# Kernel optimization log

Measured on AMD Instinct MI355X. Metric: run time of the kernel, lower is better.

The kernel has to match this reference:

```python
import jax, jax.numpy as jnp
import numpy as np

N = 50000
E = 800000
D = 256        # encoder_dim; also hidden*heads for both layers
H = 4          # heads
C = 64         # hidden_dim per head
OUT = 5        # classes
NEG_SLOPE = 0.2
GN_EPS = 1e-5
SM_EPS = 1e-16  # PyG softmax denominator epsilon


def setup_inputs() -> dict:
    key = jax.random.key(0)
    ks = jax.random.split(key, 20)
    sc = lambda fan_in: 1.0 / np.sqrt(fan_in)
    inp = {
        "x": jax.random.normal(ks[0], (N, D), dtype=jnp.float32),
        "edge_index": jax.random.randint(ks[1], (2, E), 0, N, dtype=jnp.int64),
        # two GATv2 layers (stacked on leading axis): lin_l, lin_r, att, bias
        "Wl": jax.random.normal(ks[2], (2, D, H * C), dtype=jnp.float32) * sc(D),
        "Wr": jax.random.normal(ks[3], (2, D, H * C), dtype=jnp.float32) * sc(D),
        "att": jax.random.normal(ks[4], (2, H, C), dtype=jnp.float32) * sc(C),
        "bconv": jnp.zeros((2, H * C), dtype=jnp.float32),
        # parallel linear skips
        "Wlin": jax.random.normal(ks[5], (2, D, H * C), dtype=jnp.float32) * sc(D),
        "blin": jnp.zeros((2, H * C), dtype=jnp.float32),
        # GraphNorm params
        "gn_w": jnp.ones((2, H * C), dtype=jnp.float32),
        "gn_b": jnp.zeros((2, H * C), dtype=jnp.float32),
        "gn_ms": jnp.ones((2, H * C), dtype=jnp.float32),
        # final GATv2 (concat=False -> head mean, out=5) and final linear
        "fWl": jax.random.normal(ks[6], (D, H * OUT), dtype=jnp.float32) * sc(D),
        "fWr": jax.random.normal(ks[7], (D, H * OUT), dtype=jnp.float32) * sc(D),
        "fatt": jax.random.normal(ks[8], (H, OUT), dtype=jnp.float32) * sc(OUT),
        "fbconv": jnp.zeros((OUT,), dtype=jnp.float32),
        "fWlin": jax.random.normal(ks[9], (D, OUT), dtype=jnp.float32) * sc(D),
        "fblin": jnp.zeros((OUT,), dtype=jnp.float32),
    }
    return inp


def _gatv2(x, src, dst, Wl, Wr, att, heads, ch):
    # x: [N, Din]; returns [N, heads, ch]
    n = x.shape[0]
    xl = (x @ Wl).reshape(n, heads, ch)  # source messages
    xr = (x @ Wr).reshape(n, heads, ch)  # target query part
    e = jax.nn.leaky_relu(xl[src] + xr[dst], NEG_SLOPE)      # [E, H, C]
    score = jnp.einsum("ehc,hc->eh", e, att)                  # [E, H]
    # segment softmax over incoming edges of each target node
    m = jax.ops.segment_max(score, dst, num_segments=n)       # [N, H]
    a = jnp.exp(score - m[dst])
    denom = jax.ops.segment_sum(a, dst, num_segments=n)       # [N, H]
    alpha = a / (denom[dst] + SM_EPS)                         # [E, H]
    return jax.ops.segment_sum(alpha[..., None] * xl[src], dst, num_segments=n)


def _graphnorm(x, w, b, ms):
    mean = jnp.mean(x, axis=0)
    centered = x - mean * ms
    var = jnp.mean(centered * centered, axis=0)
    return w * centered * jax.lax.rsqrt(var + GN_EPS) + b


def reference(x, edge_index, Wl, Wr, att, bconv, Wlin, blin, gn_w, gn_b, gn_ms,
              fWl, fWr, fatt, fbconv, fWlin, fblin):
    src, dst = edge_index[0], edge_index[1]
    emb = x
    for i in range(2):
        cpart = _gatv2(emb, src, dst, Wl[i], Wr[i], att[i], H, C).reshape(N, H * C) + bconv[i]
        lpart = emb @ Wlin[i] + blin[i]
        cpart = _graphnorm(cpart, gn_w[i], gn_b[i], gn_ms[i])
        emb = jax.nn.elu(cpart + lpart)
    cpart = _gatv2(emb, src, dst, fWl, fWr, fatt, H, OUT).mean(axis=1) + fbconv  # concat=False
    lpart = emb @ fWlin + fblin
    return jax.nn.log_softmax(cpart + lpart, axis=1)
```

## Files before the change

kernel.cpp:

```cpp
#include <hip/hip_runtime.h>

#define NN 50000
#define EE 800000
#define DD 256
#define NB 196

typedef unsigned short u16;
typedef unsigned int u32;

typedef __attribute__((ext_vector_type(8))) short short8;
typedef __attribute__((ext_vector_type(4))) float f32x4;
typedef __attribute__((ext_vector_type(4))) unsigned short u16x4;

__device__ __forceinline__ float b2f(u16 u) {
  union { u32 i; float f; } c; c.i = ((u32)u) << 16; return c.f;
}
__device__ __forceinline__ u16 f2b(float f) {
  union { float f; u32 i; } c; c.f = f;
  u32 u = c.i;
  return (u16)((u + 0x7fffu + ((u >> 16) & 1u)) >> 16);
}
__device__ __forceinline__ float lrelu(float x) { return fmaxf(x, 0.2f * x); }
__device__ __forceinline__ float ldf(const void* p, int i, int bf) {
  return bf ? b2f(((const u16*)p)[i]) : ((const float*)p)[i];
}
__device__ __forceinline__ int lde(const void* ei, int idx, int m64) {
  int v = m64 ? (int)((const long long*)ei)[idx] : ((const int*)ei)[idx];
  return v < 0 ? 0 : (v >= NN ? NN - 1 : v);
}
__device__ __forceinline__ float cexp(float s) {
  return __expf(fminf(fmaxf(s, -60.f), 60.f));
}

__global__ __launch_bounds__(256) void init_kernel(const void* x, const void* ei,
                                                   int* flags, int* cnt) {
  int i = blockIdx.x * 256 + threadIdx.x;
  if (i < NN) cnt[i] = 0;
  if (blockIdx.x == 0 && threadIdx.x < 64) {
    int lane = threadIdx.x;
    const u16* xw = (const u16*)x;
    int c = 0;
    for (int k = lane; k < 512; k += 64) {
      u16 w = xw[k];
      int e = (w >> 7) & 0xFF;
      if ((e >= 107 && e <= 147) || (w & 0x7FFF) == 0) ++c;
    }
    const u32* ew = (const u32*)ei;
    int zc = 0;
    for (int k = 1 + 2 * lane; k < 1024; k += 128)
      if (ew[k] == 0) ++zc;
    #pragma unroll
    for (int off = 1; off < 64; off <<= 1) {
      c += __shfl_xor(c, off);
      zc += __shfl_xor(zc, off);
    }
    if (lane == 0) {
      flags[0] = (c >= 440) ? 1 : 0;
      flags[1] = (zc >= 400) ? 1 : 0;
    }
  }
}

__global__ void hist_kernel(const void* ei, const int* flags, int* cnt) {
  int e = blockIdx.x * 256 + threadIdx.x;
  if (e < EE) atomicAdd(&cnt[lde(ei, EE + e, flags[1])], 1);
}

__global__ __launch_bounds__(256) void bsum_kernel(const int* __restrict__ deg,
                                                   int* __restrict__ bsum) {
  int i = blockIdx.x * 256 + threadIdx.x;
  int v = (i < NN) ? deg[i] : 0;
  #pragma unroll
  for (int off = 1; off < 64; off <<= 1) v += __shfl_xor(v, off);
  __shared__ int ws[4];
  int lane = threadIdx.x & 63, wid = threadIdx.x >> 6;
  if (lane == 0) ws[wid] = v;
  __syncthreads();
  if (threadIdx.x == 0) bsum[blockIdx.x] = ws[0] + ws[1] + ws[2] + ws[3];
}

__global__ __launch_bounds__(256) void bscan_kernel(const int* __restrict__ bsum,
                                                    int* __restrict__ boff) {
  int t = threadIdx.x;
  int v = (t < NB) ? bsum[t] : 0;
  int iv = v;
  int lane = t & 63, wid = t >> 6;
  #pragma unroll
  for (int off = 1; off < 64; off <<= 1) {
    int u = __shfl_up(iv, off);
    if (lane >= off) iv += u;
  }
  __shared__ int ws[4];
  if (lane == 63) ws[wid] = iv;
  __syncthreads();
  int add = 0;
  for (int w = 0; w < wid; ++w) add += ws[w];
  if (t < NB) boff[t] = iv - v + add;
}

__global__ __launch_bounds__(256) void bwrite_kernel(const int* __restrict__ deg,
                                                     const int* __restrict__ boff,
                                                     int* __restrict__ rowptr) {
  int i = blockIdx.x * 256 + threadIdx.x;
  int v = (i < NN) ? deg[i] : 0;
  int iv = v;
  int lane = threadIdx.x & 63, wid = threadIdx.x >> 6;
  #pragma unroll
  for (int off = 1; off < 64; off <<= 1) {
    int u = __shfl_up(iv, off);
    if (lane >= off) iv += u;
  }
  __shared__ int ws[4];
  if (lane == 63) ws[wid] = iv;
  __syncthreads();
  int add = boff[blockIdx.x];
  for (int w = 0; w < wid; ++w) add += ws[w];
  if (i <= NN) rowptr[i] = iv - v + add;
}

__global__ void fill_kernel(const void* ei, const int* flags, const int* __restrict__ rowptr,
                            int* __restrict__ cnt, int* __restrict__ col) {
  int e = blockIdx.x * 256 + threadIdx.x;
  if (e < EE) {
    int m64 = flags[1];
    int dst = lde(ei, EE + e, m64);
    int old = atomicSub(&cnt[dst], 1);
    int pos = rowptr[dst] + old - 1;
    if (pos >= 0 && pos < EE) col[pos] = lde(ei, e, m64);
  }
}

__global__ __launch_bounds__(256) void prep_kernel(
    const void* Wl, const void* Wr, const void* Wlin,
    const void* fWl, const void* fWr, const void* fWlin,
    const void* x, const int* flags, u16* wpack, u16* fwp, u16* xb) {
  int bf = flags[0];
  int bid = blockIdx.x;
  if (bid < 1536) {
    int idx = bid * 256 + threadIdx.x;
    int m = idx >> 16, e = idx & 65535;
    int layer = (m >= 3) ? 1 : 0, sel = m - layer * 3;
    const void* src = (sel == 0 ? Wl : (sel == 1 ? Wr : Wlin));
    int k = e >> 8, n = e & 255;
    wpack[(m << 16) + ((((k >> 3) << 8) + n) << 3) + (k & 7)] =
        f2b(ldf(src, layer * 65536 + e, bf));
  } else if (bid < 1584) {
    int idx = (bid - 1536) * 256 + threadIdx.x;
    int j = idx & 7;
    int col = (idx >> 3) % 48;
    int kk = idx / (48 * 8);
    int k = kk * 8 + j;
    float v = 0.f;
    if (col < 20)      v = ldf(fWl, k * 20 + col, bf);
    else if (col < 40) v = ldf(fWr, k * 20 + (col - 20), bf);
    else if (col < 45) v = ldf(fWlin, k * 5 + (col - 40), bf);
    fwp[idx] = f2b(v);
  } else {
    int base = (bid - 1584) * 1024 + threadIdx.x * 4;
    if (bf) {
      *(u16x4*)(xb + base) = *(const u16x4*)((const u16*)x + base);
    } else {
      f32x4 s = *(const f32x4*)((const float*)x + base);
      u16x4 o;
      #pragma unroll
      for (int j = 0; j < 4; ++j) o[j] = f2b(s[j]);
      *(u16x4*)(xb + base) = o;
    }
  }
}

__global__ __launch_bounds__(256) void gemm_kernel(
    const u16* __restrict__ A, const u16* __restrict__ wpack, const void* blin,
    const int* flags, int layer, float* __restrict__ sums,
    u16* __restrict__ xl, u16* __restrict__ xr, u16* __restrict__ lp, int M) {
  __shared__ __align__(16) u16 bsh[16384];
  if (blockIdx.x == 0 && blockIdx.y == 0) {
    sums[threadIdx.x] = 0.f;
    sums[threadIdx.x + 256] = 0.f;
  }
  int wave = threadIdx.x >> 6;
  int lane = threadIdx.x & 63;
  int q = lane >> 4;
  int t = lane & 15;
  int m0 = blockIdx.x * 64 + wave * 16;
  int yh = blockIdx.y;

  int arow = m0 + t;
  if (arow >= M) arow = M - 1;
  const u16* Abase = A + (size_t)arow * DD + q * 8;
  short8 af[8];
  #pragma unroll
  for (int i = 0; i < 8; ++i) af[i] = *(const short8*)(Abase + i * 32);

  int bf = flags[0];

  for (int yi = 0; yi < 6; ++yi) {
    int y = yh * 6 + yi;
    int m = y >> 2;
    int col0 = (y & 3) * 64;
    const u16* wb = wpack + (m << 16);

    __syncthreads();
    #pragma unroll
    for (int itc = 0; itc < 8; ++itc) {
      int chunk = threadIdx.x + itc * 256;
      int kk = chunk >> 6;
      int off = chunk & 63;
      *(uint4*)&bsh[(kk << 9) + (off << 3)] =
          *(const uint4*)(wb + (((kk << 8) + col0) << 3) + (off << 3));
    }
    __syncthreads();

    f32x4 acc[4];
    #pragma unroll
    for (int ns = 0; ns < 4; ++ns) acc[ns] = (f32x4){0.f, 0.f, 0.f, 0.f};

    #pragma unroll
    for (int i = 0; i < 8; ++i) {
      int kk = i * 4 + q;
      const u16* bb = &bsh[(kk << 9) + (t << 3)];
      #pragma unroll
      for (int ns = 0; ns < 4; ++ns) {
        short8 b = *(const short8*)(bb + (ns << 7));
        acc[ns] = __builtin_amdgcn_mfma_f32_16x16x32_bf16(af[i], b, acc[ns], 0, 0, 0);
      }
    }

    u16* dstp = (y < 4) ? xl : (y < 8) ? xr : lp;
    bool isLp = (y >= 8);
    #pragma unroll
    for (int ns = 0; ns < 4; ++ns) {
      int c = col0 + ns * 16 + t;
      float bias = isLp ? ldf(blin, layer * 256 + c, bf) : 0.f;
      #pragma unroll
      for (int r = 0; r < 4; ++r) {
        int row = m0 + q * 4 + r;
        if (row < M) dstp[(size_t)row * DD + c] = f2b(acc[ns][r] + bias);
      }
    }
  }
}

__global__ __launch_bounds__(256) void fgemm_kernel(
    const u16* __restrict__ A, const u16* __restrict__ fwp, const void* fblin,
    const int* flags, float* __restrict__ zl, float* __restrict__ zr,
    float* __restrict__ lp5, int M) {
  int wave = threadIdx.x >> 6;
  int lane = threadIdx.x & 63;
  int q = lane >> 4;
  int t = lane & 15;
  int m0 = blockIdx.x * 64 + wave * 16;

  f32x4 acc[3];
  #pragma unroll
  for (int ns = 0; ns < 3; ++ns) acc[ns] = (f32x4){0.f, 0.f, 0.f, 0.f};

  int arow = m0 + t;
  if (arow >= M) arow = M - 1;
  const u16* Abase = A + (size_t)arow * DD + q * 8;

  #pragma unroll
  for (int k0 = 0; k0 < DD; k0 += 32) {
    short8 a = *(const short8*)(Abase + k0);
    int kk = (k0 >> 3) + q;
    #pragma unroll
    for (int ns = 0; ns < 3; ++ns) {
      short8 b = *(const short8*)(fwp + (((kk * 48) + ns * 16 + t) << 3));
      acc[ns] = __builtin_amdgcn_mfma_f32_16x16x32_bf16(a, b, acc[ns], 0, 0, 0);
    }
  }

  int bf = flags[0];
  #pragma unroll
  for (int ns = 0; ns < 3; ++ns) {
    int c = ns * 16 + t;
    #pragma unroll
    for (int r = 0; r < 4; ++r) {
      int row = m0 + q * 4 + r;
      if (row < M) {
        float v = acc[ns][r];
        if (c < 20)      zl[row * 20 + c] = v;
        else if (c < 40) zr[row * 20 + (c - 20)] = v;
        else if (c < 45) lp5[row * 5 + (c - 40)] = v + ldf(fblin, c - 40, bf);
      }
    }
  }
}

__device__ __forceinline__ void edge_step(u16x4 s4, const float* xrv, const float* atv,
                                          float& l, float* acc) {
  float x0 = b2f(s4[0]), x1 = b2f(s4[1]), x2 = b2f(s4[2]), x3 = b2f(s4[3]);
  float sp = atv[0] * lrelu(x0 + xrv[0]) + atv[1] * lrelu(x1 + xrv[1]) +
             atv[2] * lrelu(x2 + xrv[2]) + atv[3] * lrelu(x3 + xrv[3]);
  sp += __shfl_xor(sp, 1);
  sp += __shfl_xor(sp, 2);
  sp += __shfl_xor(sp, 4);
  sp += __shfl_xor(sp, 8);
  float pz = cexp(sp);
  l += pz;
  acc[0] += pz * x0;
  acc[1] += pz * x1;
  acc[2] += pz * x2;
  acc[3] += pz * x3;
}

__global__ __launch_bounds__(256) void agg_kernel(
    const u16* __restrict__ xl, const u16* __restrict__ xr,
    const int* __restrict__ rowptr, const int* __restrict__ col,
    const void* att, const void* bconv, const int* flags, int layer,
    u16* __restrict__ cpart) {
  int wave = threadIdx.x >> 6;
  int node = blockIdx.x * 4 + wave;
  int lane = threadIdx.x & 63;
  int h = lane >> 4;
  int cb = (lane & 15) * 4;
  int base = h * 64 + cb;
  int bf = flags[0];

  u16x4 r4 = *(const u16x4*)(xr + (size_t)node * DD + base);
  float xrv[4], atv[4];
  #pragma unroll
  for (int j = 0; j < 4; ++j) {
    xrv[j] = b2f(r4[j]);
    atv[j] = ldf(att, layer * 256 + base + j, bf);
  }

  float l = 0.f;
  float acc[4] = {0.f, 0.f, 0.f, 0.f};
  int e0 = rowptr[node], e1 = rowptr[node + 1];
  const u16* xlp = xl + base;

  int e = e0;
  for (; e + 4 <= e1; e += 4) {
    int s0 = col[e], s1 = col[e + 1], s2 = col[e + 2], s3 = col[e + 3];
    u16x4 v0 = *(const u16x4*)(xlp + (size_t)s0 * DD);
    u16x4 v1 = *(const u16x4*)(xlp + (size_t)s1 * DD);
    u16x4 v2 = *(const u16x4*)(xlp + (size_t)s2 * DD);
    u16x4 v3 = *(const u16x4*)(xlp + (size_t)s3 * DD);
    edge_step(v0, xrv, atv, l, acc);
    edge_step(v1, xrv, atv, l, acc);
    edge_step(v2, xrv, atv, l, acc);
    edge_step(v3, xrv, atv, l, acc);
  }
  for (; e < e1; ++e) {
    u16x4 v = *(const u16x4*)(xlp + (size_t)col[e] * DD);
    edge_step(v, xrv, atv, l, acc);
  }

  float inv = 1.f / (l + 1e-16f);
  u16x4 outw;
  #pragma unroll
  for (int j = 0; j < 4; ++j)
    outw[j] = f2b(acc[j] * inv + ldf(bconv, layer * 256 + base + j, bf));
  *(u16x4*)(cpart + (size_t)node * DD + base) = outw;
}

__global__ __launch_bounds__(256) void stats_kernel(const u16* __restrict__ cpart,
                                                    float* __restrict__ sums) {
  int ch = threadIdx.x;
  int n0 = blockIdx.x * 100, n1 = n0 + 100;
  float s = 0.f, s2 = 0.f;
  for (int n = n0; n < n1; ++n) {
    float x = b2f(cpart[(size_t)n * DD + ch]);
    s += x; s2 += x * x;
  }
  atomicAdd(&sums[ch], s);
  atomicAdd(&sums[256 + ch], s2);
}

__global__ __launch_bounds__(256) void norm_kernel(
    const u16* __restrict__ cpart, const u16* __restrict__ lp,
    const void* gw, const void* gb, const void* gms, const int* flags, int layer,
    const float* __restrict__ sums, u16* __restrict__ emb) {
  int t = threadIdx.x;
  int node = blockIdx.x * 4 + (t >> 6);
  int c4 = (t & 63) * 4;
  int bf = flags[0];
  size_t idx = (size_t)node * DD + c4;
  const float invN = 1.f / (float)NN;
  u16x4 cp = *(const u16x4*)(cpart + idx);
  u16x4 lv = *(const u16x4*)(lp + idx);
  u16x4 o;
  #pragma unroll
  for (int j = 0; j < 4; ++j) {
    int ch = c4 + j;
    float mean = sums[ch] * invN;
    float ex2 = sums[256 + ch] * invN;
    float mm = mean * ldf(gms, layer * 256 + ch, bf);
    float var = ex2 - 2.f * mm * mean + mm * mm;
    float x = b2f(cp[j]);
    float y = ldf(gw, layer * 256 + ch, bf) * (x - mm) * rsqrtf(fmaxf(var, 0.f) + 1e-5f) +
              ldf(gb, layer * 256 + ch, bf) + b2f(lv[j]);
    o[j] = f2b(y > 0.f ? y : expm1f(y));
  }
  *(u16x4*)(emb + idx) = o;
}

__global__ __launch_bounds__(256) void finagg_kernel(
    const float* __restrict__ zl, const float* __restrict__ zr,
    const int* __restrict__ rowptr, const int* __restrict__ col,
    const void* fatt, const void* fbconv, const int* flags,
    const float* __restrict__ lp5, void* outv) {
  int node = blockIdx.x * 4 + (threadIdx.x >> 6);
  int lane = threadIdx.x & 63;
  int bf = flags[0];
  int h = lane >> 4, sub = lane & 15;

  float zrv[5], atv[5];
  #pragma unroll
  for (int c = 0; c < 5; ++c) {
    zrv[c] = zr[node * 20 + h * 5 + c];
    atv[c] = ldf(fatt, h * 5 + c, bf);
  }
  float l = 0.f, acc[5] = {0.f, 0.f, 0.f, 0.f, 0.f};
  int e0 = rowptr[node], e1 = rowptr[node + 1];
  for (int e = e0 + sub; e < e1; e += 16) {
    int src = col[e];
    const float* zs = zl + src * 20 + h * 5;
    float zlv[5];
    #pragma unroll
    for (int c = 0; c < 5; ++c) zlv[c] = zs[c];
    float s = 0.f;
    #pragma unroll
    for (int c = 0; c < 5; ++c) s += atv[c] * lrelu(zlv[c] + zrv[c]);
    float pz = cexp(s);
    l += pz;
    #pragma unroll
    for (int c = 0; c < 5; ++c) acc[c] += pz * zlv[c];
  }
  #pragma unroll
  for (int off = 1; off < 16; off <<= 1) {
    l += __shfl_xor(l, off);
    #pragma unroll
    for (int c = 0; c < 5; ++c) acc[c] += __shfl_xor(acc[c], off);
  }
  float inv = 1.f / (l + 1e-16f);
  float v[5];
  #pragma unroll
  for (int c = 0; c < 5; ++c) {
    float tv = acc[c] * inv;
    tv += __shfl_xor(tv, 16);
    tv += __shfl_xor(tv, 32);
    v[c] = tv * 0.25f;
  }
  if (lane == 0) {
    float mx = -3.0e38f;
    #pragma unroll
    for (int c = 0; c < 5; ++c) {
      v[c] += ldf(fbconv, c, bf) + lp5[node * 5 + c];
      mx = fmaxf(mx, v[c]);
    }
    float se = 0.f;
    #pragma unroll
    for (int c = 0; c < 5; ++c) se += __expf(v[c] - mx);
    float lse = mx + __logf(se);
    #pragma unroll
    for (int c = 0; c < 5; ++c) {
      float r = v[c] - lse;
      if (bf) ((u16*)outv)[node * 5 + c] = f2b(r);
      else    ((float*)outv)[node * 5 + c] = r;
    }
  }
}

extern "C" void kernel_launch(void* const* d_in, const int* in_sizes, int n_in,
                              void* d_out, int out_size, void* d_ws, size_t ws_size,
                              hipStream_t stream) {
  (void)in_sizes; (void)n_in; (void)out_size; (void)ws_size;
  const void* x     = d_in[0];
  const void* ei    = d_in[1];
  const void* Wl    = d_in[2];
  const void* Wr    = d_in[3];
  const void* att   = d_in[4];
  const void* bconv = d_in[5];
  const void* Wlin  = d_in[6];
  const void* blin  = d_in[7];
  const void* gnw   = d_in[8];
  const void* gnb   = d_in[9];
  const void* gnms  = d_in[10];
  const void* fWl   = d_in[11];
  const void* fWr   = d_in[12];
  const void* fatt  = d_in[13];
  const void* fbc   = d_in[14];
  const void* fWlin = d_in[15];
  const void* fblin = d_in[16];

  char* p = (char*)d_ws;
  auto take = [&](size_t bytes) {
    char* r = p;
    p += (bytes + 511) & ~(size_t)511;
    return r;
  };
  int* flags   = (int*)take(512);
  int* rowptr  = (int*)take((NN + 1) * sizeof(int));
  int* cnt     = (int*)take(NN * sizeof(int));
  int* colx    = (int*)take(EE * sizeof(int));
  int* bsum    = (int*)take(256 * sizeof(int));
  int* boff    = (int*)take(256 * sizeof(int));
  u16* wpack   = (u16*)take((size_t)6 * 65536 * sizeof(u16));
  u16* fwp     = (u16*)take((size_t)32 * 48 * 8 * sizeof(u16));
  float* sums  = (float*)take(512 * sizeof(float));
  char* unionA = take((size_t)NN * DD * 4);
  u16* xb      = (u16*)unionA;
  u16* cpart   = (u16*)unionA;
  float* zl    = (float*)unionA;
  float* zr    = (float*)(unionA + (size_t)NN * 20 * 4);
  float* lp5   = (float*)(unionA + (size_t)NN * 40 * 4);
  u16* xl      = (u16*)take((size_t)NN * DD * 2);
  u16* xr      = (u16*)take((size_t)NN * DD * 2);
  u16* lp      = (u16*)take((size_t)NN * DD * 2);
  u16* emb     = (u16*)take((size_t)NN * DD * 2);

  init_kernel<<<dim3(NB), dim3(256), 0, stream>>>(x, ei, flags, cnt);
  hist_kernel<<<dim3((EE + 255) / 256), dim3(256), 0, stream>>>(ei, flags, cnt);
  bsum_kernel<<<dim3(NB), dim3(256), 0, stream>>>(cnt, bsum);
  bscan_kernel<<<dim3(1), dim3(256), 0, stream>>>(bsum, boff);
  bwrite_kernel<<<dim3(NB), dim3(256), 0, stream>>>(cnt, boff, rowptr);
  fill_kernel<<<dim3((EE + 255) / 256), dim3(256), 0, stream>>>(ei, flags, rowptr, cnt, colx);
  prep_kernel<<<dim3(1584 + NN * DD / 1024), dim3(256), 0, stream>>>(
      Wl, Wr, Wlin, fWl, fWr, fWlin, x, flags, wpack, fwp, xb);

  const u16* layerin = xb;
  for (int i = 0; i < 2; ++i) {
    gemm_kernel<<<dim3((NN + 63) / 64, 2), dim3(256), 0, stream>>>(
        layerin, wpack + (size_t)i * 3 * 65536, blin, flags, i, sums, xl, xr, lp, NN);
    agg_kernel<<<dim3(NN / 4), dim3(256), 0, stream>>>(xl, xr, rowptr, colx, att, bconv,
                                                       flags, i, cpart);
    stats_kernel<<<dim3(500), dim3(256), 0, stream>>>(cpart, sums);
    norm_kernel<<<dim3(NN / 4), dim3(256), 0, stream>>>(cpart, lp, gnw, gnb, gnms, flags, i,
                                                        sums, emb);
    layerin = emb;
  }
  fgemm_kernel<<<dim3((NN + 63) / 64), dim3(256), 0, stream>>>(emb, fwp, fblin, flags,
                                                               zl, zr, lp5, NN);
  finagg_kernel<<<dim3(NN / 4), dim3(256), 0, stream>>>(zl, zr, rowptr, colx, fatt, fbc,
                                                        flags, lp5, d_out);
}
```

Measured before the change: 661.5 us.

## Use packed FP32 math, vectorized col loads, and direct-to-LDS weight loads

The aggregation kernel's per-edge math now uses v_pk_add/mul/fma_f32 packed instructions, and the exp clamp uses med3. The edge loop first runs scalar until e is 4-aligned, then reads four column indices with one 16-byte load and computes addresses with 32-bit byte offsets. The GEMM's weight staging into shared memory now uses global_load_lds (direct global-to-LDS) instead of register round-trips. These changes aim to cut ALU instruction count and load/address overhead, at the cost of inline asm that constrains the compiler's scheduling and 32-bit offset arithmetic that relies on the node count staying small.

```diff
diff --git a/kernel.cpp b/kernel.cpp
--- a/kernel.cpp
+++ b/kernel.cpp
@@ -10,7 +10,9 @@
 
 typedef __attribute__((ext_vector_type(8))) short short8;
 typedef __attribute__((ext_vector_type(4))) float f32x4;
+typedef __attribute__((ext_vector_type(2))) float f32x2;
 typedef __attribute__((ext_vector_type(4))) unsigned short u16x4;
+typedef __attribute__((ext_vector_type(4))) int i32x4;
 
 __device__ __forceinline__ float b2f(u16 u) {
   union { u32 i; float f; } c; c.i = ((u32)u) << 16; return c.f;
@@ -29,7 +31,23 @@
   return v < 0 ? 0 : (v >= NN ? NN - 1 : v);
 }
 __device__ __forceinline__ float cexp(float s) {
-  return __expf(fminf(fmaxf(s, -60.f), 60.f));
+  return __expf(__builtin_amdgcn_fmed3f(s, -60.f, 60.f));
+}
+
+__device__ __forceinline__ f32x2 pk_add(f32x2 a, f32x2 b) {
+  f32x2 d; asm("v_pk_add_f32 %0, %1, %2" : "=v"(d) : "v"(a), "v"(b)); return d;
+}
+__device__ __forceinline__ f32x2 pk_mul(f32x2 a, f32x2 b) {
+  f32x2 d; asm("v_pk_mul_f32 %0, %1, %2" : "=v"(d) : "v"(a), "v"(b)); return d;
+}
+__device__ __forceinline__ f32x2 pk_fma(f32x2 a, f32x2 b, f32x2 c) {
+  f32x2 d; asm("v_pk_fma_f32 %0, %1, %2, %3" : "=v"(d) : "v"(a), "v"(b), "v"(c)); return d;
+}
+
+__device__ __forceinline__ void gload_lds16(const void* g, void* l) {
+  __builtin_amdgcn_global_load_lds(
+      (const __attribute__((address_space(1))) void*)g,
+      (__attribute__((address_space(3))) void*)l, 16, 0, 0);
 }
 
 __global__ __launch_bounds__(256) void init_kernel(const void* x, const void* ei,
@@ -203,11 +221,10 @@
     __syncthreads();
     #pragma unroll
     for (int itc = 0; itc < 8; ++itc) {
-      int chunk = threadIdx.x + itc * 256;
-      int kk = chunk >> 6;
-      int off = chunk & 63;
-      *(uint4*)&bsh[(kk << 9) + (off << 3)] =
-          *(const uint4*)(wb + (((kk << 8) + col0) << 3) + (off << 3));
+      int kk = wave + itc * 4;
+      const u16* gp = wb + (((kk << 8) + col0) << 3) + (lane << 3);
+      u16* lb = &bsh[(wave * 64 + itc * 256) << 3];
+      gload_lds16(gp, lb);
     }
     __syncthreads();
 
@@ -287,21 +304,33 @@
   }
 }
 
-__device__ __forceinline__ void edge_step(u16x4 s4, const float* xrv, const float* atv,
-                                          float& l, float* acc) {
-  float x0 = b2f(s4[0]), x1 = b2f(s4[1]), x2 = b2f(s4[2]), x3 = b2f(s4[3]);
-  float sp = atv[0] * lrelu(x0 + xrv[0]) + atv[1] * lrelu(x1 + xrv[1]) +
-             atv[2] * lrelu(x2 + xrv[2]) + atv[3] * lrelu(x3 + xrv[3]);
+struct AggCtx {
+  f32x2 xr01, xr23, at01, at23, c02;
+};
+
+__device__ __forceinline__ void edge_step2(u16x4 s4, const AggCtx& C, float& l,
+                                           f32x2& a01, f32x2& a23) {
+  f32x2 x01, x23;
+  x01.x = b2f(s4[0]); x01.y = b2f(s4[1]);
+  x23.x = b2f(s4[2]); x23.y = b2f(s4[3]);
+  f32x2 y01 = pk_add(x01, C.xr01);
+  f32x2 y23 = pk_add(x23, C.xr23);
+  f32x2 t01 = pk_mul(y01, C.c02);
+  f32x2 t23 = pk_mul(y23, C.c02);
+  f32x2 m01, m23;
+  m01.x = fmaxf(y01.x, t01.x); m01.y = fmaxf(y01.y, t01.y);
+  m23.x = fmaxf(y23.x, t23.x); m23.y = fmaxf(y23.y, t23.y);
+  f32x2 sp2 = pk_fma(C.at23, m23, pk_mul(C.at01, m01));
+  float sp = sp2.x + sp2.y;
   sp += __shfl_xor(sp, 1);
   sp += __shfl_xor(sp, 2);
   sp += __shfl_xor(sp, 4);
   sp += __shfl_xor(sp, 8);
   float pz = cexp(sp);
   l += pz;
-  acc[0] += pz * x0;
-  acc[1] += pz * x1;
-  acc[2] += pz * x2;
-  acc[3] += pz * x3;
+  f32x2 pzp; pzp.x = pz; pzp.y = pz;
+  a01 = pk_fma(pzp, x01, a01);
+  a23 = pk_fma(pzp, x23, a23);
 }
 
 __global__ __launch_bounds__(256) void agg_kernel(
@@ -318,40 +347,47 @@
   int bf = flags[0];
 
   u16x4 r4 = *(const u16x4*)(xr + (size_t)node * DD + base);
-  float xrv[4], atv[4];
-  #pragma unroll
-  for (int j = 0; j < 4; ++j) {
-    xrv[j] = b2f(r4[j]);
-    atv[j] = ldf(att, layer * 256 + base + j, bf);
-  }
+  AggCtx C;
+  C.xr01.x = b2f(r4[0]); C.xr01.y = b2f(r4[1]);
+  C.xr23.x = b2f(r4[2]); C.xr23.y = b2f(r4[3]);
+  C.at01.x = ldf(att, layer * 256 + base + 0, bf);
+  C.at01.y = ldf(att, layer * 256 + base + 1, bf);
+  C.at23.x = ldf(att, layer * 256 + base + 2, bf);
+  C.at23.y = ldf(att, layer * 256 + base + 3, bf);
+  C.c02.x = 0.2f; C.c02.y = 0.2f;
 
   float l = 0.f;
-  float acc[4] = {0.f, 0.f, 0.f, 0.f};
+  f32x2 a01 = {0.f, 0.f}, a23 = {0.f, 0.f};
   int e0 = rowptr[node], e1 = rowptr[node + 1];
-  const u16* xlp = xl + base;
+  const char* xlb = (const char*)xl;
+  u32 baseb = (u32)(base << 1);
+
+  auto do_edge = [&](int c) {
+    u32 off = ((u32)c << 9) + baseb;
+    edge_step2(*(const u16x4*)(xlb + off), C, l, a01, a23);
+  };
 
   int e = e0;
+  for (; e < e1 && (e & 3); ++e) do_edge(col[e]);
   for (; e + 4 <= e1; e += 4) {
-    int s0 = col[e], s1 = col[e + 1], s2 = col[e + 2], s3 = col[e + 3];
-    u16x4 v0 = *(const u16x4*)(xlp + (size_t)s0 * DD);
-    u16x4 v1 = *(const u16x4*)(xlp + (size_t)s1 * DD);
-    u16x4 v2 = *(const u16x4*)(xlp + (size_t)s2 * DD);
-    u16x4 v3 = *(const u16x4*)(xlp + (size_t)s3 * DD);
-    edge_step(v0, xrv, atv, l, acc);
-    edge_step(v1, xrv, atv, l, acc);
-    edge_step(v2, xrv, atv, l, acc);
-    edge_step(v3, xrv, atv, l, acc);
-  }
-  for (; e < e1; ++e) {
-    u16x4 v = *(const u16x4*)(xlp + (size_t)col[e] * DD);
-    edge_step(v, xrv, atv, l, acc);
-  }
+    i32x4 cq = *(const i32x4*)(col + e);
+    u16x4 v0 = *(const u16x4*)(xlb + (((u32)cq.x << 9) + baseb));
+    u16x4 v1 = *(const u16x4*)(xlb + (((u32)cq.y << 9) + baseb));
+    u16x4 v2 = *(const u16x4*)(xlb + (((u32)cq.z << 9) + baseb));
+    u16x4 v3 = *(const u16x4*)(xlb + (((u32)cq.w << 9) + baseb));
+    edge_step2(v0, C, l, a01, a23);
+    edge_step2(v1, C, l, a01, a23);
+    edge_step2(v2, C, l, a01, a23);
+    edge_step2(v3, C, l, a01, a23);
+  }
+  for (; e < e1; ++e) do_edge(col[e]);
 
   float inv = 1.f / (l + 1e-16f);
+  float av[4] = {a01.x, a01.y, a23.x, a23.y};
   u16x4 outw;
   #pragma unroll
   for (int j = 0; j < 4; ++j)
-    outw[j] = f2b(acc[j] * inv + ldf(bconv, layer * 256 + base + j, bf));
+    outw[j] = f2b(av[j] * inv + ldf(bconv, layer * 256 + base + j, bf));
   *(u16x4*)(cpart + (size_t)node * DD + base) = outw;
 }
 
```

Result: slower. 692.3 us (+4.7%).

## Use DPP reductions, direct-to-LDS loads, vectorized index loads and padded final layouts

Applied to the files above, without the earlier changes.

Several independent micro-optimizations land together. The per-edge 16-lane score reduction now uses DPP row operations instead of shuffles, and the clamp uses fmed3. The GEMM weight tile is staged with global_load_lds instead of going through registers. The aggregation loop fetches four column indices in one vector load and uses 32-bit byte offsets. The final-layer zl/zr/lp5 buffers are padded to 8-float strides per head so they can be read with vector loads. These changes target instruction count and memory-access efficiency, at the cost of extra footprint in the padded buffers and an alignment prologue in the edge loop.

```diff
diff --git a/kernel.cpp b/kernel.cpp
--- a/kernel.cpp
+++ b/kernel.cpp
@@ -11,6 +11,7 @@
 typedef __attribute__((ext_vector_type(8))) short short8;
 typedef __attribute__((ext_vector_type(4))) float f32x4;
 typedef __attribute__((ext_vector_type(4))) unsigned short u16x4;
+typedef __attribute__((ext_vector_type(4))) int i32x4;
 
 __device__ __forceinline__ float b2f(u16 u) {
   union { u32 i; float f; } c; c.i = ((u32)u) << 16; return c.f;
@@ -29,7 +30,28 @@
   return v < 0 ? 0 : (v >= NN ? NN - 1 : v);
 }
 __device__ __forceinline__ float cexp(float s) {
-  return __expf(fminf(fmaxf(s, -60.f), 60.f));
+  return __expf(__builtin_amdgcn_fmed3f(s, -60.f, 60.f));
+}
+
+template <int CTRL>
+__device__ __forceinline__ float dpp_add(float s) {
+  union { float f; int i; } a, b;
+  a.f = s;
+  b.i = __builtin_amdgcn_update_dpp(0, a.i, CTRL, 0xf, 0xf, true);
+  return s + b.f;
+}
+__device__ __forceinline__ float row16_allsum(float s) {
+  s = dpp_add<0xB1>(s);
+  s = dpp_add<0x4E>(s);
+  s = dpp_add<0x141>(s);
+  s = dpp_add<0x140>(s);
+  return s;
+}
+
+__device__ __forceinline__ void gload_lds16(const void* g, void* l) {
+  __builtin_amdgcn_global_load_lds(
+      (const __attribute__((address_space(1))) void*)g,
+      (__attribute__((address_space(3))) void*)l, 16, 0, 0);
 }
 
 __global__ __launch_bounds__(256) void init_kernel(const void* x, const void* ei,
@@ -203,11 +225,10 @@
     __syncthreads();
     #pragma unroll
     for (int itc = 0; itc < 8; ++itc) {
-      int chunk = threadIdx.x + itc * 256;
-      int kk = chunk >> 6;
-      int off = chunk & 63;
-      *(uint4*)&bsh[(kk << 9) + (off << 3)] =
-          *(const uint4*)(wb + (((kk << 8) + col0) << 3) + (off << 3));
+      int kk = wave + itc * 4;
+      const u16* gp = wb + (((kk << 8) + col0) << 3) + (lane << 3);
+      u16* lb = &bsh[(wave * 64 + itc * 256) << 3];
+      gload_lds16(gp, lb);
     }
     __syncthreads();
 
@@ -279,9 +300,14 @@
       int row = m0 + q * 4 + r;
       if (row < M) {
         float v = acc[ns][r];
-        if (c < 20)      zl[row * 20 + c] = v;
-        else if (c < 40) zr[row * 20 + (c - 20)] = v;
-        else if (c < 45) lp5[row * 5 + (c - 40)] = v + ldf(fblin, c - 40, bf);
+        if (c < 20) {
+          zl[row * 32 + (c / 5) * 8 + (c % 5)] = v;
+        } else if (c < 40) {
+          int c2 = c - 20;
+          zr[row * 32 + (c2 / 5) * 8 + (c2 % 5)] = v;
+        } else if (c < 45) {
+          lp5[row * 8 + (c - 40)] = v + ldf(fblin, c - 40, bf);
+        }
       }
     }
   }
@@ -292,10 +318,7 @@
   float x0 = b2f(s4[0]), x1 = b2f(s4[1]), x2 = b2f(s4[2]), x3 = b2f(s4[3]);
   float sp = atv[0] * lrelu(x0 + xrv[0]) + atv[1] * lrelu(x1 + xrv[1]) +
              atv[2] * lrelu(x2 + xrv[2]) + atv[3] * lrelu(x3 + xrv[3]);
-  sp += __shfl_xor(sp, 1);
-  sp += __shfl_xor(sp, 2);
-  sp += __shfl_xor(sp, 4);
-  sp += __shfl_xor(sp, 8);
+  sp = row16_allsum(sp);
   float pz = cexp(sp);
   l += pz;
   acc[0] += pz * x0;
@@ -328,22 +351,27 @@
   float l = 0.f;
   float acc[4] = {0.f, 0.f, 0.f, 0.f};
   int e0 = rowptr[node], e1 = rowptr[node + 1];
-  const u16* xlp = xl + base;
+  const char* xlb = (const char*)xl;
+  u32 baseb = (u32)(base << 1);
 
   int e = e0;
+  for (; e < e1 && (e & 3); ++e) {
+    u16x4 v = *(const u16x4*)(xlb + (((u32)col[e] << 9) + baseb));
+    edge_step(v, xrv, atv, l, acc);
+  }
   for (; e + 4 <= e1; e += 4) {
-    int s0 = col[e], s1 = col[e + 1], s2 = col[e + 2], s3 = col[e + 3];
-    u16x4 v0 = *(const u16x4*)(xlp + (size_t)s0 * DD);
-    u16x4 v1 = *(const u16x4*)(xlp + (size_t)s1 * DD);
-    u16x4 v2 = *(const u16x4*)(xlp + (size_t)s2 * DD);
-    u16x4 v3 = *(const u16x4*)(xlp + (size_t)s3 * DD);
+    i32x4 cq = *(const i32x4*)(col + e);
+    u16x4 v0 = *(const u16x4*)(xlb + (((u32)cq.x << 9) + baseb));
+    u16x4 v1 = *(const u16x4*)(xlb + (((u32)cq.y << 9) + baseb));
+    u16x4 v2 = *(const u16x4*)(xlb + (((u32)cq.z << 9) + baseb));
+    u16x4 v3 = *(const u16x4*)(xlb + (((u32)cq.w << 9) + baseb));
     edge_step(v0, xrv, atv, l, acc);
     edge_step(v1, xrv, atv, l, acc);
     edge_step(v2, xrv, atv, l, acc);
     edge_step(v3, xrv, atv, l, acc);
   }
   for (; e < e1; ++e) {
-    u16x4 v = *(const u16x4*)(xlp + (size_t)col[e] * DD);
+    u16x4 v = *(const u16x4*)(xlb + (((u32)col[e] << 9) + baseb));
     edge_step(v, xrv, atv, l, acc);
   }
 
@@ -406,20 +434,21 @@
   int bf = flags[0];
   int h = lane >> 4, sub = lane & 15;
 
-  float zrv[5], atv[5];
-  #pragma unroll
-  for (int c = 0; c < 5; ++c) {
-    zrv[c] = zr[node * 20 + h * 5 + c];
-    atv[c] = ldf(fatt, h * 5 + c, bf);
-  }
+  const float* zrp = zr + node * 32 + h * 8;
+  f32x4 zr4 = *(const f32x4*)zrp;
+  float zrv[5] = {zr4.x, zr4.y, zr4.z, zr4.w, zrp[4]};
+  float atv[5];
+  #pragma unroll
+  for (int c = 0; c < 5; ++c) atv[c] = ldf(fatt, h * 5 + c, bf);
+
   float l = 0.f, acc[5] = {0.f, 0.f, 0.f, 0.f, 0.f};
   int e0 = rowptr[node], e1 = rowptr[node + 1];
   for (int e = e0 + sub; e < e1; e += 16) {
     int src = col[e];
-    const float* zs = zl + src * 20 + h * 5;
-    float zlv[5];
-    #pragma unroll
-    for (int c = 0; c < 5; ++c) zlv[c] = zs[c];
+    const float* zs = zl + src * 32 + h * 8;
+    f32x4 z4 = *(const f32x4*)zs;
+    float z4s = zs[4];
+    float zlv[5] = {z4.x, z4.y, z4.z, z4.w, z4s};
     float s = 0.f;
     #pragma unroll
     for (int c = 0; c < 5; ++c) s += atv[c] * lrelu(zlv[c] + zrv[c]);
@@ -447,7 +476,7 @@
     float mx = -3.0e38f;
     #pragma unroll
     for (int c = 0; c < 5; ++c) {
-      v[c] += ldf(fbconv, c, bf) + lp5[node * 5 + c];
+      v[c] += ldf(fbconv, c, bf) + lp5[node * 8 + c];
       mx = fmaxf(mx, v[c]);
     }
     float se = 0.f;
@@ -504,8 +533,8 @@
   u16* xb      = (u16*)unionA;
   u16* cpart   = (u16*)unionA;
   float* zl    = (float*)unionA;
-  float* zr    = (float*)(unionA + (size_t)NN * 20 * 4);
-  float* lp5   = (float*)(unionA + (size_t)NN * 40 * 4);
+  float* zr    = (float*)(unionA + (size_t)NN * 32 * 4);
+  float* lp5   = (float*)(unionA + (size_t)NN * 64 * 4);
   u16* xl      = (u16*)take((size_t)NN * DD * 2);
   u16* xr      = (u16*)take((size_t)NN * DD * 2);
   u16* lp      = (u16*)take((size_t)NN * DD * 2);
```

Measured after the change: 656.0 us. No clear change (-0.8%).
